# Kernel optimization log

Measured on AMD Instinct MI355X. Metric: run time of the kernel, lower is better.

## Reference

```python
import jax, jax.numpy as jnp
import numpy as np

B, T, D, H, F = 2, 2048, 1024, 16, 4096
DH = D // H  # 64
EPS = 1e-5


def setup_inputs() -> dict:
    key = jax.random.key(0)
    ks = jax.random.split(key, 12)
    s = 0.02
    return {
        "embedding": jax.random.normal(ks[0], (B, T, D), dtype=jnp.float32),
        "Wq": jax.random.normal(ks[1], (H, D, DH), dtype=jnp.float32) * s,
        "Wk": jax.random.normal(ks[2], (H, D, DH), dtype=jnp.float32) * s,
        "Wv": jax.random.normal(ks[3], (H, D, DH), dtype=jnp.float32) * s,
        "Wo": jax.random.normal(ks[4], (D, D), dtype=jnp.float32) * s,
        "bo": jnp.zeros((D,), dtype=jnp.float32),
        "W1": jax.random.normal(ks[5], (D, F), dtype=jnp.float32) * s,
        "b1": jnp.zeros((F,), dtype=jnp.float32),
        "W2": jax.random.normal(ks[6], (F, D), dtype=jnp.float32) * s,
        "b2": jnp.zeros((D,), dtype=jnp.float32),
        "g1": jnp.ones((D,), dtype=jnp.float32),
        "be1": jnp.zeros((D,), dtype=jnp.float32),
        "g2": jnp.ones((D,), dtype=jnp.float32),
        "be2": jnp.zeros((D,), dtype=jnp.float32),
    }


def _layernorm(x, g, b):
    mu = jnp.mean(x, axis=-1, keepdims=True)
    var = jnp.mean(jnp.square(x - mu), axis=-1, keepdims=True)
    return (x - mu) * jax.lax.rsqrt(var + EPS) * g + b


def reference(embedding, Wq, Wk, Wv, Wo, bo, W1, b1, W2, b2, g1, be1, g2, be2):
    x = embedding  # [B, T, D]
    # per-head projections (no bias), stacked: [B, H, T, DH]
    q = jnp.einsum("btd,hde->bhte", x, Wq)
    k = jnp.einsum("btd,hde->bhte", x, Wk)
    v = jnp.einsum("btd,hde->bhte", x, Wv)
    scores = jnp.einsum("bhte,bhse->bhts", q, k)  # [B, H, T, T]
    mask = jnp.tril(jnp.ones((T, T), dtype=bool))
    # Original masks to -inf first, then scales; -inf * scale = -inf, so this
    # equals softmax(scale * scores) on the causal support.
    scale = DH ** (-0.5)
    scores = jnp.where(mask, scores * scale, -jnp.inf)
    attn = jax.nn.softmax(scores, axis=-1)
    o = jnp.einsum("bhts,bhse->bthe", attn, v).reshape(B, T, D)  # head concat
    attn_out = o @ Wo + bo
    a = x + _layernorm(attn_out, g1, be1)  # residual uses original input
    f = jax.nn.relu(a @ W1 + b1) @ W2 + b2
    out = x + _layernorm(f, g2, be2)  # NOTE: residual from x, as in source
    return out
```

## Files before the change

kernel.cpp:

```cpp
#include <hip/hip_runtime.h>
#include <hip/hip_bf16.h>


#define Bq_ 2
#define T_ 2048
#define D_ 1024
#define H_ 16
#define DH_ 64
#define F_ 4096
#define N_ (Bq_ * T_)
#define EPS_ 1e-5f
#define KP 72

typedef __hip_bfloat16 bf16;
typedef unsigned short u16;
typedef __attribute__((ext_vector_type(8))) short bfrag;
typedef __attribute__((ext_vector_type(4))) float f32x4;

__device__ __forceinline__ u16 f2b(float f) {
    bf16 h = __float2bfloat16(f);
    return *(u16*)&h;
}
__device__ __forceinline__ float b2f_bits(u16 u) {
    return __uint_as_float(((unsigned)u) << 16);
}

__device__ __forceinline__ int swz(int row, int col) {
    return (col & ~31) | ((((col >> 3) ^ (row >> 1)) & 3) << 3) | (col & 7);
}

template <int N>
__device__ __forceinline__ void vmwait() {
    asm volatile("s_waitcnt vmcnt(%0)" :: "i"(N) : "memory");
}

#define GLDS16(g, l) __builtin_amdgcn_global_load_lds( \
    (const __attribute__((address_space(1))) unsigned int*)(g), \
    (__attribute__((address_space(3))) unsigned int*)(l), 16, 0, 0)

__device__ __forceinline__ void tc_body(
    float (*Ts)[65], const float* s, int spitch,
    u16* dst, int dpitch, int drow0, int kcol0)
{
    const int t = threadIdx.x;
    #pragma unroll
    for (int i = 0; i < 4; i++) {
        const int idx = t + i * 256;
        const int kk = idx >> 4;
        const int mm = (idx & 15) * 4;
        float4 v = *(const float4*)(s + (size_t)kk * spitch + mm);
        Ts[mm][kk] = v.x; Ts[mm + 1][kk] = v.y;
        Ts[mm + 2][kk] = v.z; Ts[mm + 3][kk] = v.w;
    }
    __syncthreads();
    const int mm = t >> 2;
    const int kk0 = (t & 3) * 16;
    u16 o[16];
    #pragma unroll
    for (int j = 0; j < 16; j++) o[j] = f2b(Ts[mm][kk0 + j]);
    const int dr = drow0 + mm;
    u16* drow = dst + (size_t)dr * dpitch;
    const int c0 = kcol0 + kk0;
    *(uint4*)&drow[swz(dr, c0)]     = *(uint4*)&o[0];
    *(uint4*)&drow[swz(dr, c0 + 8)] = *(uint4*)&o[8];
}

__global__ __launch_bounds__(256) void tcvt(
    const float* __restrict__ src, int spitch, int srow0, int scol0,
    u16* __restrict__ dst, int dpitch, int drow0)
{
    __shared__ float Ts[64][65];
    const int mb = blockIdx.x, kb = blockIdx.y;
    const float* s = src + (size_t)(srow0 + kb * 64) * spitch + scol0 + mb * 64;
    tc_body(Ts, s, spitch, dst, dpitch, drow0 + mb * 64, kb * 64);
}

__global__ __launch_bounds__(256) void tcvt_kv(
    const float* __restrict__ Wk, const float* __restrict__ Wv,
    u16* __restrict__ dst)
{
    __shared__ float Ts[64][65];
    const int kb = blockIdx.y, z = blockIdx.z;
    const int sel = z >> 4, zz = z & 15;
    const float* src = sel ? Wv : Wk;
    const float* s = src + (size_t)zz * 1024 * 64 + (size_t)(kb * 64) * 64;
    tc_body(Ts, s, 64, dst, 1024, sel * 1024 + zz * 64, kb * 64);
}

__global__ __launch_bounds__(256) void tcvt_ffn(
    const float* __restrict__ W1, const float* __restrict__ W2, int c,
    u16* __restrict__ W1T, u16* __restrict__ W2T)
{
    __shared__ float Ts[64][65];
    const int mb = blockIdx.x, kb = blockIdx.y, z = blockIdx.z;
    const float* src = z ? W2 : W1;
    const int spitch = z ? 1024 : 4096;
    const int srow0  = z ? c * 1024 : 0;
    const int scol0  = z ? 0 : c * 1024;
    u16* dst = z ? W2T : W1T;
    const float* s = src + (size_t)(srow0 + kb * 64) * spitch + scol0 + mb * 64;
    tc_body(Ts, s, spitch, dst, 1024, mb * 64, kb * 64);
}

template <int AF32, int SPLIT, int RELU, int ACC, int NT, int CSWZ, int WAVE>
__global__ __launch_bounds__(256) void cgemm(
    const void* __restrict__ A, int lda,
    const u16* __restrict__ BT,
    u16* __restrict__ C0, u16* __restrict__ C1, int ldc,
    int Kdim,
    const float* __restrict__ bias, int bias_off)
{
    static_assert(NT == 2 || NT == 4, "NT");
    static_assert(!AF32 || NT == 4, "AF32 path assumes BN=128");
    static_assert(!(AF32 && WAVE), "WAVE requires glds-only staging");
    constexpr int BN = NT * 32;
    constexpr int NBUF = (NT == 2) ? 5 : 4;
    constexpr int DPT  = NBUF - 1;
    constexpr int LPT  = 4 + NT;
    constexpr int BELEM = 64 * 32;
    constexpr int AELEM = NT * 16 * 32;
    constexpr int PBUF  = BELEM + AELEM;
    constexpr int SELEM = WAVE ? 4 * NBUF * PBUF
                               : 2 * BN * 32 + 2 * 128 * 32;
    __shared__ alignas(16) u16 SMEM[SELEM];

    const int tid = threadIdx.x;
    const int lane = tid & 63;
    const int w = tid >> 6;
    const int lo16 = lane & 15;
    const int quad = lane >> 4;
    const int wi = w >> 1, wj = w & 1;

    const int m0 = blockIdx.x * 128;
    const int n0 = blockIdx.y * BN;

    f32x4 acc[NT][4] = {};

    const int c8 = (lane & 3) * 8;
    const int r4 = lane >> 2;
    const int fcol = ((quad ^ ((lo16 >> 1) & 3)) << 3);

    const int nsteps = Kdim >> 5;

    if constexpr (WAVE) {
        const u16* Ab = (const u16*)A;
        u16* wbase = &SMEM[w * NBUF * PBUF];
        auto wstage = [&](int slot, int k0) {
            u16* bb = wbase + slot * PBUF;
            #pragma unroll
            for (int c = 0; c < 4; c++)
                GLDS16(BT + (size_t)(m0 + wj * 64 + c * 16 + r4) * Kdim + k0 + c8,
                       bb + c * 512);
            u16* ab = bb + BELEM;
            #pragma unroll
            for (int c = 0; c < NT; c++)
                GLDS16(Ab + (size_t)(n0 + wi * (NT * 16) + c * 16 + r4) * lda + k0 + c8,
                       ab + c * 512);
        };
        #pragma unroll
        for (int i = 0; i < DPT; i++) wstage(i, i * 32);
        int t = 0, cb = 0;
        for (; t + DPT <= nsteps; ++t) {
            vmwait<(DPT - 1) * LPT>();
            __builtin_amdgcn_sched_barrier(0);
            const u16* bb = wbase + cb * PBUF;
            const u16* ab = bb + BELEM;
            bfrag af[NT], bfv[4];
            #pragma unroll
            for (int it = 0; it < NT; it++)
                af[it] = *(const bfrag*)(ab + (it * 16 + lo16) * 32 + fcol);
            #pragma unroll
            for (int jt = 0; jt < 4; jt++)
                bfv[jt] = *(const bfrag*)(bb + (jt * 16 + lo16) * 32 + fcol);
            if (t + DPT < nsteps)
                wstage(cb == 0 ? NBUF - 1 : cb - 1, (t + DPT) * 32);
            __builtin_amdgcn_s_setprio(1);
            #pragma unroll
            for (int it = 0; it < NT; it++)
                #pragma unroll
                for (int jt = 0; jt < 4; jt++)
                    acc[it][jt] = __builtin_amdgcn_mfma_f32_16x16x32_bf16(
                        af[it], bfv[jt], acc[it][jt], 0, 0, 0);
            __builtin_amdgcn_s_setprio(0);
            cb = (cb + 1 == NBUF) ? 0 : cb + 1;
        }
        vmwait<0>();
        __builtin_amdgcn_sched_barrier(0);
        for (; t < nsteps; ++t) {
            const u16* bb = wbase + cb * PBUF;
            const u16* ab = bb + BELEM;
            bfrag af[NT], bfv[4];
            #pragma unroll
            for (int it = 0; it < NT; it++)
                af[it] = *(const bfrag*)(ab + (it * 16 + lo16) * 32 + fcol);
            #pragma unroll
            for (int jt = 0; jt < 4; jt++)
                bfv[jt] = *(const bfrag*)(bb + (jt * 16 + lo16) * 32 + fcol);
            #pragma unroll
            for (int it = 0; it < NT; it++)
                #pragma unroll
                for (int jt = 0; jt < 4; jt++)
                    acc[it][jt] = __builtin_amdgcn_mfma_f32_16x16x32_bf16(
                        af[it], bfv[jt], acc[it][jt], 0, 0, 0);
            cb = (cb + 1 == NBUF) ? 0 : cb + 1;
        }
    } else {
        u16* As_ = SMEM;
        u16* Bs_ = SMEM + 2 * BN * 32;
        const int br0 = w * 32 + r4;
        const int br1 = br0 + 16;
        auto stage = [&](int buf, int k0) {
            GLDS16(BT + (size_t)(m0 + br0) * Kdim + k0 + c8,
                   Bs_ + buf * 128 * 32 + (w * 2 + 0) * 512);
            GLDS16(BT + (size_t)(m0 + br1) * Kdim + k0 + c8,
                   Bs_ + buf * 128 * 32 + (w * 2 + 1) * 512);
            const int ar = tid >> 1;
            const int kh = (tid & 1) * 16;
            const float* ap = (const float*)A + (size_t)(n0 + ar) * lda + k0 + kh;
            float4 v0 = ((const float4*)ap)[0];
            float4 v1 = ((const float4*)ap)[1];
            float4 v2 = ((const float4*)ap)[2];
            float4 v3 = ((const float4*)ap)[3];
            uint4 a0, a1;
            a0.x = (unsigned)f2b(v0.x) | ((unsigned)f2b(v0.y) << 16);
            a0.y = (unsigned)f2b(v0.z) | ((unsigned)f2b(v0.w) << 16);
            a0.z = (unsigned)f2b(v1.x) | ((unsigned)f2b(v1.y) << 16);
            a0.w = (unsigned)f2b(v1.z) | ((unsigned)f2b(v1.w) << 16);
            a1.x = (unsigned)f2b(v2.x) | ((unsigned)f2b(v2.y) << 16);
            a1.y = (unsigned)f2b(v2.z) | ((unsigned)f2b(v2.w) << 16);
            a1.z = (unsigned)f2b(v3.x) | ((unsigned)f2b(v3.y) << 16);
            a1.w = (unsigned)f2b(v3.z) | ((unsigned)f2b(v3.w) << 16);
            u16* arow = As_ + buf * BN * 32 + ar * 32;
            *(uint4*)&arow[swz(ar, kh)] = a0;
            *(uint4*)&arow[swz(ar, kh + 8)] = a1;
        };
        stage(0, 0);
        __syncthreads();
        int cur = 0;
        for (int t = 0; t < nsteps; ++t) {
            if (t + 1 < nsteps) stage(cur ^ 1, (t + 1) * 32);
            bfrag af[NT], bfv[4];
            #pragma unroll
            for (int it = 0; it < NT; it++)
                af[it] = *(const bfrag*)(As_ + cur * BN * 32
                         + (wi * (NT * 16) + it * 16 + lo16) * 32 + fcol);
            #pragma unroll
            for (int jt = 0; jt < 4; jt++)
                bfv[jt] = *(const bfrag*)(Bs_ + cur * 128 * 32
                          + (wj * 64 + jt * 16 + lo16) * 32 + fcol);
            __builtin_amdgcn_s_setprio(1);
            #pragma unroll
            for (int it = 0; it < NT; it++)
                #pragma unroll
                for (int jt = 0; jt < 4; jt++)
                    acc[it][jt] = __builtin_amdgcn_mfma_f32_16x16x32_bf16(
                        af[it], bfv[jt], acc[it][jt], 0, 0, 0);
            __builtin_amdgcn_s_setprio(0);
            if (t + 1 < nsteps) {
                __syncthreads();
                cur ^= 1;
            }
        }
    }
    #pragma unroll
    for (int jt = 0; jt < 4; jt++) {
        const int col = m0 + wj * 64 + jt * 16 + lo16;
        u16* Cp;
        int cc;
        if constexpr (SPLIT) {
            Cp = (col >> 10) ? C1 : C0;
            cc = col & 1023;
        } else {
            Cp = C0;
            cc = col;
        }
        const float bv = bias ? bias[bias_off + col] : 0.f;
        #pragma unroll
        for (int it = 0; it < NT; it++) {
            #pragma unroll
            for (int r = 0; r < 4; r++) {
                const int row = n0 + wi * (NT * 16) + it * 16 + quad * 4 + r;
                float v = acc[it][jt][r] + bv;
                if constexpr (RELU) v = fmaxf(v, 0.f);
                const int ccs = CSWZ ? swz(row, cc) : cc;
                u16* cp = Cp + (size_t)row * ldc + ccs;
                if constexpr (ACC) v += b2f_bits(*cp);
                *cp = f2b(v);
            }
        }
    }
}

template <int AF32, int QKV, int RELU, int ACC>
__global__ __launch_bounds__(256) void mgemm(
    const void* __restrict__ A,
    const float* __restrict__ B0f, const float* __restrict__ B1f, const float* __restrict__ B2f,
    u16* __restrict__ C0, u16* __restrict__ C1, u16* __restrict__ C2,
    int ldb, int brow_off, int bcol_off,
    const float* __restrict__ bias, int bias_off)
{
    __shared__ alignas(16) u16 As[128][32];
    __shared__ alignas(16) u16 Bt[128][40];
    __shared__ alignas(16) float Bs32[32][132];

    const int tid = threadIdx.x;
    const int lane = tid & 63;
    const int w = tid >> 6;
    const int lo16 = lane & 15;
    const int quad = lane >> 4;
    const int wi = w >> 1, wj = w & 1;

    const int m0 = blockIdx.x * 128;
    const int n0 = blockIdx.y * 128;

    f32x4 acc[4][4] = {};

    const int ar  = tid >> 1;
    const int akh = (tid & 1) * 16;
    const int bmq = tid & 31;
    const int bkb = (tid >> 5) * 4;
    const int tm  = tid >> 1;
    const int tkh = (tid & 1) * 16;

    for (int k0 = 0; k0 < 1024; k0 += 32) {
        uint4 a0, a1;
        if constexpr (AF32) {
            const float* ap = (const float*)A + (size_t)(n0 + ar) * 1024 + k0 + akh;
            float4 v0 = ((const float4*)ap)[0];
            float4 v1 = ((const float4*)ap)[1];
            float4 v2 = ((const float4*)ap)[2];
            float4 v3 = ((const float4*)ap)[3];
            a0.x = (unsigned)f2b(v0.x) | ((unsigned)f2b(v0.y) << 16);
            a0.y = (unsigned)f2b(v0.z) | ((unsigned)f2b(v0.w) << 16);
            a0.z = (unsigned)f2b(v1.x) | ((unsigned)f2b(v1.y) << 16);
            a0.w = (unsigned)f2b(v1.z) | ((unsigned)f2b(v1.w) << 16);
            a1.x = (unsigned)f2b(v2.x) | ((unsigned)f2b(v2.y) << 16);
            a1.y = (unsigned)f2b(v2.z) | ((unsigned)f2b(v2.w) << 16);
            a1.z = (unsigned)f2b(v3.x) | ((unsigned)f2b(v3.y) << 16);
            a1.w = (unsigned)f2b(v3.z) | ((unsigned)f2b(v3.w) << 16);
        } else {
            const u16* ap = (const u16*)A + (size_t)(n0 + ar) * 1024 + k0 + akh;
            a0 = ((const uint4*)ap)[0];
            a1 = ((const uint4*)ap)[1];
        }
        #pragma unroll
        for (int kk = 0; kk < 4; kk++) {
            const int k = bkb + kk;
            const float* bp;
            if constexpr (QKV) {
                const int m = m0 + bmq * 4;
                const int sel = m >> 10;
                const int mm = m & 1023;
                const float* Wp = (sel == 0) ? B0f : ((sel == 1) ? B1f : B2f);
                bp = Wp + ((size_t)(mm >> 6) * 1024 + k0 + k) * 64 + (mm & 63);
            } else {
                bp = B0f + (size_t)(brow_off + k0 + k) * ldb + bcol_off + m0 + bmq * 4;
            }
            *(float4*)&Bs32[k][bmq * 4] = *(const float4*)bp;
        }
        __syncthreads();
        *(uint4*)&As[ar][akh] = a0;
        *(uint4*)&As[ar][akh + 8] = a1;
        {
            u16 t[16];
            #pragma unroll
            for (int i = 0; i < 16; i++) t[i] = f2b(Bs32[tkh + i][tm]);
            *(uint4*)&Bt[tm][tkh] = *(uint4*)&t[0];
            *(uint4*)&Bt[tm][tkh + 8] = *(uint4*)&t[8];
        }
        __syncthreads();
        bfrag af[4], bfv[4];
        #pragma unroll
        for (int it = 0; it < 4; it++)
            af[it] = *(const bfrag*)&As[wi * 64 + it * 16 + lo16][quad * 8];
        #pragma unroll
        for (int jt = 0; jt < 4; jt++)
            bfv[jt] = *(const bfrag*)&Bt[wj * 64 + jt * 16 + lo16][quad * 8];
        #pragma unroll
        for (int it = 0; it < 4; it++)
            #pragma unroll
            for (int jt = 0; jt < 4; jt++)
                acc[it][jt] = __builtin_amdgcn_mfma_f32_16x16x32_bf16(
                    af[it], bfv[jt], acc[it][jt], 0, 0, 0);
        __syncthreads();
    }
    #pragma unroll
    for (int jt = 0; jt < 4; jt++) {
        const int col = m0 + wj * 64 + jt * 16 + lo16;
        u16* Cp;
        int cc;
        if constexpr (QKV) {
            const int sel = col >> 10;
            cc = col & 1023;
            Cp = (sel == 0) ? C0 : ((sel == 1) ? C1 : C2);
        } else {
            Cp = C0;
            cc = col;
        }
        const float bv = bias ? bias[bias_off + col] : 0.f;
        #pragma unroll
        for (int it = 0; it < 4; it++) {
            #pragma unroll
            for (int r = 0; r < 4; r++) {
                const int row = n0 + wi * 64 + it * 16 + quad * 4 + r;
                float v = acc[it][jt][r] + bv;
                if constexpr (RELU) v = fmaxf(v, 0.f);
                u16* cp = Cp + (size_t)row * 1024 + cc;
                if constexpr (ACC) v += b2f_bits(*cp);
                *cp = f2b(v);
            }
        }
    }
}

__global__ __launch_bounds__(256) void fattn_kernel(
    u16* __restrict__ Q, const u16* __restrict__ Kg, const u16* __restrict__ Vg)
{
    const int bo_ = blockIdx.x;
    const int bi = ((bo_ & 7) << 6) | (bo_ >> 3);
    const int qp = bi & 15;
    const int h  = (bi >> 4) & 15;
    const int b  = bi >> 8;
    const int tid = threadIdx.x;
    const int w = tid >> 6;
    const int lane = tid & 63;
    const int lo16 = lane & 15;
    const int quad = lane >> 4;

    __shared__ alignas(16) u16 Ks[64][KP];
    __shared__ alignas(16) u16 Vt[64][KP];
    __shared__ alignas(16) u16 Ps[4][16][KP];

    const int sr = tid >> 2;
    const int ec = (tid & 3) * 16;

    #pragma unroll 1
    for (int pi = 0; pi < 2; pi++) {
        const int qt = pi ? (31 - qp) : qp;
        const int q0 = qt * 64;
        const size_t qrow = (size_t)(b * T_ + q0 + w * 16 + lo16) * 1024 + h * 64;
        bfrag qa0 = *(const bfrag*)(Q + qrow + quad * 8);
        bfrag qa1 = *(const bfrag*)(Q + qrow + 32 + quad * 8);

        f32x4 oacc[4] = {};
        float m_r[4], l_r[4];
        #pragma unroll
        for (int r = 0; r < 4; r++) { m_r[r] = -3e38f; l_r[r] = 0.f; }

        uint4 ka, kb, va, vb;
        {
            const size_t grow = (size_t)(b * T_ + sr) * 1024 + h * 64 + ec;
            ka = *(const uint4*)(Kg + grow);
            kb = *(const uint4*)(Kg + grow + 8);
            va = *(const uint4*)(Vg + grow);
            vb = *(const uint4*)(Vg + grow + 8);
        }

        for (int st = 0; st <= qt; st++) {
            *(uint4*)&Ks[sr][ec] = ka;
            *(uint4*)&Ks[sr][ec + 8] = kb;
            {
                unsigned vv[8] = {va.x, va.y, va.z, va.w, vb.x, vb.y, vb.z, vb.w};
                #pragma unroll
                for (int k2 = 0; k2 < 8; k2++) {
                    Vt[ec + 2 * k2][sr]     = (u16)(vv[k2] & 0xffff);
                    Vt[ec + 2 * k2 + 1][sr] = (u16)(vv[k2] >> 16);
                }
            }
            __syncthreads();
            if (st < qt) {
                const size_t grow = (size_t)(b * T_ + (st + 1) * 64 + sr) * 1024
                                  + h * 64 + ec;
                ka = *(const uint4*)(Kg + grow);
                kb = *(const uint4*)(Kg + grow + 8);
                va = *(const uint4*)(Vg + grow);
                vb = *(const uint4*)(Vg + grow + 8);
            }

            float sv[4][4];
            #pragma unroll
            for (int nt = 0; nt < 4; nt++) {
                bfrag kb0 = *(const bfrag*)&Ks[nt * 16 + lo16][quad * 8];
                bfrag kb1 = *(const bfrag*)&Ks[nt * 16 + lo16][32 + quad * 8];
                f32x4 cs = {0.f, 0.f, 0.f, 0.f};
                cs = __builtin_amdgcn_mfma_f32_16x16x32_bf16(qa0, kb0, cs, 0, 0, 0);
                cs = __builtin_amdgcn_mfma_f32_16x16x32_bf16(qa1, kb1, cs, 0, 0, 0);
                #pragma unroll
                for (int r = 0; r < 4; r++) sv[nt][r] = cs[r] * 0.125f;
            }
            if (st == qt) {
                #pragma unroll
                for (int nt = 0; nt < 4; nt++)
                    #pragma unroll
                    for (int r = 0; r < 4; r++)
                        if (nt * 16 + lo16 > w * 16 + quad * 4 + r) sv[nt][r] = -3e38f;
            }
            #pragma unroll
            for (int r = 0; r < 4; r++) {
                float m = fmaxf(fmaxf(sv[0][r], sv[1][r]), fmaxf(sv[2][r], sv[3][r]));
                #pragma unroll
                for (int off = 1; off < 16; off <<= 1)
                    m = fmaxf(m, __shfl_xor(m, off, 64));
                float mnew = fmaxf(m_r[r], m);
                float alpha = __expf(m_r[r] - mnew);
                m_r[r] = mnew;
                float s = 0.f;
                #pragma unroll
                for (int nt = 0; nt < 4; nt++) {
                    sv[nt][r] = __expf(sv[nt][r] - mnew);
                    s += sv[nt][r];
                }
                #pragma unroll
                for (int off = 1; off < 16; off <<= 1)
                    s += __shfl_xor(s, off, 64);
                l_r[r] = l_r[r] * alpha + s;
                #pragma unroll
                for (int et = 0; et < 4; et++) oacc[et][r] *= alpha;
            }
            #pragma unroll
            for (int nt = 0; nt < 4; nt++)
                #pragma unroll
                for (int r = 0; r < 4; r++)
                    Ps[w][quad * 4 + r][nt * 16 + lo16] = f2b(sv[nt][r]);
            bfrag pa0 = *(const bfrag*)&Ps[w][lo16][quad * 8];
            bfrag pa1 = *(const bfrag*)&Ps[w][lo16][32 + quad * 8];
            #pragma unroll
            for (int et = 0; et < 4; et++) {
                bfrag vb0 = *(const bfrag*)&Vt[et * 16 + lo16][quad * 8];
                bfrag vb1 = *(const bfrag*)&Vt[et * 16 + lo16][32 + quad * 8];
                oacc[et] = __builtin_amdgcn_mfma_f32_16x16x32_bf16(pa0, vb0, oacc[et], 0, 0, 0);
                oacc[et] = __builtin_amdgcn_mfma_f32_16x16x32_bf16(pa1, vb1, oacc[et], 0, 0, 0);
            }
            __syncthreads();
        }
        #pragma unroll
        for (int r = 0; r < 4; r++) {
            float rl = 1.f / l_r[r];
            const int row = q0 + w * 16 + quad * 4 + r;
            u16* orow = Q + (size_t)(b * T_ + row) * 1024;
            #pragma unroll
            for (int et = 0; et < 4; et++)
                orow[swz(row, h * 64 + et * 16 + lo16)] = f2b(oacc[et][r] * rl);
        }
    }
}

template <int WF32, int OSWZ>
__global__ __launch_bounds__(256) void ln_kernel(
    const u16* __restrict__ src, const float* __restrict__ resid,
    const float* __restrict__ g, const float* __restrict__ be,
    u16* __restrict__ dstb, float* __restrict__ dstf)
{
    const int r = blockIdx.x;
    const int tid = threadIdx.x;
    uint2 raw = ((const uint2*)(src + (size_t)r * D_))[tid];
    float y[4];
    y[0] = __uint_as_float(raw.x << 16);
    y[1] = __uint_as_float(raw.x & 0xffff0000u);
    y[2] = __uint_as_float(raw.y << 16);
    y[3] = __uint_as_float(raw.y & 0xffff0000u);
    float s = y[0] + y[1] + y[2] + y[3];
    float sq = y[0]*y[0] + y[1]*y[1] + y[2]*y[2] + y[3]*y[3];
    #pragma unroll
    for (int o = 32; o > 0; o >>= 1) {
        s += __shfl_down(s, o, 64);
        sq += __shfl_down(sq, o, 64);
    }
    __shared__ float rs[4], rq[4];
    if ((tid & 63) == 0) { rs[tid >> 6] = s; rq[tid >> 6] = sq; }
    __syncthreads();
    const float S = rs[0] + rs[1] + rs[2] + rs[3];
    const float Qm = rq[0] + rq[1] + rq[2] + rq[3];
    const float mu = S * (1.f / (float)D_);
    const float var = fmaxf(Qm * (1.f / (float)D_) - mu * mu, 0.f);
    const float rstd = rsqrtf(var + EPS_);
    const int c = tid * 4;
    #pragma unroll
    for (int i = 0; i < 4; i++) {
        y[i] = (y[i] - mu) * rstd * g[c + i] + be[c + i]
             + resid[(size_t)r * D_ + c + i];
    }
    if constexpr (WF32) {
        float4 o = {y[0], y[1], y[2], y[3]};
        ((float4*)(dstf + (size_t)r * D_))[tid] = o;
    } else {
        uint2 o;
        o.x = (unsigned)f2b(y[0]) | ((unsigned)f2b(y[1]) << 16);
        o.y = (unsigned)f2b(y[2]) | ((unsigned)f2b(y[3]) << 16);
        const int cs = OSWZ ? swz(r, c) : c;
        *(uint2*)(dstb + (size_t)r * D_ + cs) = o;
    }
}

extern "C" void kernel_launch(void* const* d_in, const int* in_sizes, int n_in,
                              void* d_out, int out_size, void* d_ws, size_t ws_size,
                              hipStream_t stream)
{
    const float* emb = (const float*)d_in[0];
    const float* Wq  = (const float*)d_in[1];
    const float* Wk  = (const float*)d_in[2];
    const float* Wv  = (const float*)d_in[3];
    const float* Wo  = (const float*)d_in[4];
    const float* bo  = (const float*)d_in[5];
    const float* W1  = (const float*)d_in[6];
    const float* b1  = (const float*)d_in[7];
    const float* W2  = (const float*)d_in[8];
    const float* b2  = (const float*)d_in[9];
    const float* g1  = (const float*)d_in[10];
    const float* be1 = (const float*)d_in[11];
    const float* g2  = (const float*)d_in[12];
    const float* be2 = (const float*)d_in[13];

    u16* WS = (u16*)d_ws;
    u16* DO = (u16*)d_out;

    const size_t M1 = 1024 * 1024;
    u16* WkvT = WS;
    u16* Q    = WS;
    u16* Kb   = DO;
    u16* Vb   = DO + 4 * M1;
    u16* O    = WS;
    u16* WoT  = DO;
    u16* P    = DO + 4 * M1;
    u16* Af   = DO;
    u16* Hc   = DO + 4 * M1;
    u16* W1T  = DO + 6 * M1;
    u16* W2T  = DO + 7 * M1;
    u16* F    = WS;
    float* outf = (float*)d_out;

    const dim3 blk(256);

    tcvt_kv<<<dim3(1, 16, 32), blk, 0, stream>>>(Wk, Wv, WkvT);
    cgemm<1, 1, 0, 0, 4, 0, 0><<<dim3(16, 32), blk, 0, stream>>>(
        emb, 1024, WkvT, Kb, Vb, 1024, 1024, nullptr, 0);
    mgemm<1, 1, 0, 0><<<dim3(8, 32), blk, 0, stream>>>(
        emb, Wq, Wq, Wq, Q, nullptr, nullptr, 0, 0, 0, nullptr, 0);
    fattn_kernel<<<Bq_ * H_ * 16, blk, 0, stream>>>(Q, Kb, Vb);
    tcvt<<<dim3(16, 16), blk, 0, stream>>>(Wo, 1024, 0, 0, WoT, 1024, 0);
    cgemm<0, 0, 0, 0, 4, 0, 1><<<dim3(8, 32), blk, 0, stream>>>(
        O, 1024, WoT, P, nullptr, 1024, 1024, bo, 0);
    ln_kernel<0, 1><<<N_, blk, 0, stream>>>(P, emb, g1, be1, Af, nullptr);
    for (int c = 0; c < 4; c++) {
        tcvt_ffn<<<dim3(16, 16, 2), blk, 0, stream>>>(W1, W2, c, W1T, W2T);
        for (int rh = 0; rh < 2; rh++) {
            u16* Afh = Af + (size_t)rh * 2048 * 1024;
            u16* Fh  = F  + (size_t)rh * 2048 * 1024;
            cgemm<0, 0, 1, 0, 2, 1, 1><<<dim3(8, 32), blk, 0, stream>>>(
                Afh, 1024, W1T, Hc, nullptr, 1024, 1024, b1, c * 1024);
            if (c == 0) {
                cgemm<0, 0, 0, 0, 2, 0, 1><<<dim3(8, 32), blk, 0, stream>>>(
                    Hc, 1024, W2T, Fh, nullptr, 1024, 1024, b2, 0);
            } else {
                cgemm<0, 0, 0, 1, 2, 0, 1><<<dim3(8, 32), blk, 0, stream>>>(
                    Hc, 1024, W2T, Fh, nullptr, 1024, 1024, nullptr, 0);
            }
        }
    }
    ln_kernel<1, 0><<<N_, blk, 0, stream>>>(F, emb, g2, be2, nullptr, outf);
}
```

Baseline: 558.5 us.

## Share K/V tiles across paired query tiles and remap GEMM blocks per XCD

The attention kernel previously handled its two paired query tiles (qp and 31-qp) one after the other, loading the K/V prefix twice. It now runs one loop over the longer prefix and processes both query tiles against each staged K/V tile, so the shorter tile's K/V loads are shared. This roughly halves K/V global traffic and LDS staging for those steps, at the cost of more live registers for two accumulator sets. Separately, both GEMM kernels remap block indices so consecutive blocks dispatched to the same XCD cover neighbouring tiles, aiming for better L2 locality.

```diff
diff --git a/kernel.cpp b/kernel.cpp
--- a/kernel.cpp
+++ b/kernel.cpp
@@ -37,6 +37,13 @@
 #define GLDS16(g, l) __builtin_amdgcn_global_load_lds( \
     (const __attribute__((address_space(1))) unsigned int*)(g), \
     (__attribute__((address_space(3))) unsigned int*)(l), 16, 0, 0)
+
+__device__ __forceinline__ void xcd_remap(int gx, int& bx, int& by) {
+    const int bid = blockIdx.x + gx * blockIdx.y;
+    const int t8 = bid >> 3;
+    bx = t8 % gx;
+    by = (bid & 7) + 8 * (t8 / gx);
+}
 
 __device__ __forceinline__ void tc_body(
     float (*Ts)[65], const float* s, int spitch,
@@ -131,8 +138,10 @@
     const int quad = lane >> 4;
     const int wi = w >> 1, wj = w & 1;
 
-    const int m0 = blockIdx.x * 128;
-    const int n0 = blockIdx.y * BN;
+    int bx, by;
+    xcd_remap(gridDim.x, bx, by);
+    const int m0 = bx * 128;
+    const int n0 = by * BN;
 
     f32x4 acc[NT][4] = {};
 
@@ -310,8 +319,10 @@
     const int quad = lane >> 4;
     const int wi = w >> 1, wj = w & 1;
 
-    const int m0 = blockIdx.x * 128;
-    const int n0 = blockIdx.y * 128;
+    int bx, by;
+    xcd_remap(gridDim.x, bx, by);
+    const int m0 = bx * 128;
+    const int n0 = by * 128;
 
     f32x4 acc[4][4] = {};
 
@@ -434,113 +445,124 @@
     const int sr = tid >> 2;
     const int ec = (tid & 3) * 16;
 
-    #pragma unroll 1
-    for (int pi = 0; pi < 2; pi++) {
-        const int qt = pi ? (31 - qp) : qp;
-        const int q0 = qt * 64;
-        const size_t qrow = (size_t)(b * T_ + q0 + w * 16 + lo16) * 1024 + h * 64;
-        bfrag qa0 = *(const bfrag*)(Q + qrow + quad * 8);
-        bfrag qa1 = *(const bfrag*)(Q + qrow + 32 + quad * 8);
-
-        f32x4 oacc[4] = {};
-        float m_r[4], l_r[4];
-        #pragma unroll
-        for (int r = 0; r < 4; r++) { m_r[r] = -3e38f; l_r[r] = 0.f; }
-
-        uint4 ka, kb, va, vb;
+    const int qtA = qp, qtB = 31 - qp;
+
+    const size_t qrowA = (size_t)(b * T_ + qtA * 64 + w * 16 + lo16) * 1024 + h * 64;
+    const size_t qrowB = (size_t)(b * T_ + qtB * 64 + w * 16 + lo16) * 1024 + h * 64;
+    bfrag qaA0 = *(const bfrag*)(Q + qrowA + quad * 8);
+    bfrag qaA1 = *(const bfrag*)(Q + qrowA + 32 + quad * 8);
+    bfrag qaB0 = *(const bfrag*)(Q + qrowB + quad * 8);
+    bfrag qaB1 = *(const bfrag*)(Q + qrowB + 32 + quad * 8);
+
+    f32x4 oaccA[4] = {}, oaccB[4] = {};
+    float mA[4], lA[4], mB[4], lB[4];
+    #pragma unroll
+    for (int r = 0; r < 4; r++) { mA[r] = mB[r] = -3e38f; lA[r] = lB[r] = 0.f; }
+
+    uint4 ka, kb, va, vb;
+    {
+        const size_t grow = (size_t)(b * T_ + sr) * 1024 + h * 64 + ec;
+        ka = *(const uint4*)(Kg + grow);
+        kb = *(const uint4*)(Kg + grow + 8);
+        va = *(const uint4*)(Vg + grow);
+        vb = *(const uint4*)(Vg + grow + 8);
+    }
+
+    auto proc = [&](bfrag q0f, bfrag q1f, f32x4* oacc, float* m_r, float* l_r,
+                    int qt, int st) {
+        float sv[4][4];
+        #pragma unroll
+        for (int nt = 0; nt < 4; nt++) {
+            bfrag kb0 = *(const bfrag*)&Ks[nt * 16 + lo16][quad * 8];
+            bfrag kb1 = *(const bfrag*)&Ks[nt * 16 + lo16][32 + quad * 8];
+            f32x4 cs = {0.f, 0.f, 0.f, 0.f};
+            cs = __builtin_amdgcn_mfma_f32_16x16x32_bf16(q0f, kb0, cs, 0, 0, 0);
+            cs = __builtin_amdgcn_mfma_f32_16x16x32_bf16(q1f, kb1, cs, 0, 0, 0);
+            #pragma unroll
+            for (int r = 0; r < 4; r++) sv[nt][r] = cs[r] * 0.125f;
+        }
+        if (st == qt) {
+            #pragma unroll
+            for (int nt = 0; nt < 4; nt++)
+                #pragma unroll
+                for (int r = 0; r < 4; r++)
+                    if (nt * 16 + lo16 > w * 16 + quad * 4 + r) sv[nt][r] = -3e38f;
+        }
+        #pragma unroll
+        for (int r = 0; r < 4; r++) {
+            float m = fmaxf(fmaxf(sv[0][r], sv[1][r]), fmaxf(sv[2][r], sv[3][r]));
+            #pragma unroll
+            for (int off = 1; off < 16; off <<= 1)
+                m = fmaxf(m, __shfl_xor(m, off, 64));
+            float mnew = fmaxf(m_r[r], m);
+            float alpha = __expf(m_r[r] - mnew);
+            m_r[r] = mnew;
+            float s = 0.f;
+            #pragma unroll
+            for (int nt = 0; nt < 4; nt++) {
+                sv[nt][r] = __expf(sv[nt][r] - mnew);
+                s += sv[nt][r];
+            }
+            #pragma unroll
+            for (int off = 1; off < 16; off <<= 1)
+                s += __shfl_xor(s, off, 64);
+            l_r[r] = l_r[r] * alpha + s;
+            #pragma unroll
+            for (int et = 0; et < 4; et++) oacc[et][r] *= alpha;
+        }
+        #pragma unroll
+        for (int nt = 0; nt < 4; nt++)
+            #pragma unroll
+            for (int r = 0; r < 4; r++)
+                Ps[w][quad * 4 + r][nt * 16 + lo16] = f2b(sv[nt][r]);
+        bfrag pa0 = *(const bfrag*)&Ps[w][lo16][quad * 8];
+        bfrag pa1 = *(const bfrag*)&Ps[w][lo16][32 + quad * 8];
+        #pragma unroll
+        for (int et = 0; et < 4; et++) {
+            bfrag vb0 = *(const bfrag*)&Vt[et * 16 + lo16][quad * 8];
+            bfrag vb1 = *(const bfrag*)&Vt[et * 16 + lo16][32 + quad * 8];
+            oacc[et] = __builtin_amdgcn_mfma_f32_16x16x32_bf16(pa0, vb0, oacc[et], 0, 0, 0);
+            oacc[et] = __builtin_amdgcn_mfma_f32_16x16x32_bf16(pa1, vb1, oacc[et], 0, 0, 0);
+        }
+    };
+
+    for (int st = 0; st <= qtB; st++) {
+        *(uint4*)&Ks[sr][ec] = ka;
+        *(uint4*)&Ks[sr][ec + 8] = kb;
         {
-            const size_t grow = (size_t)(b * T_ + sr) * 1024 + h * 64 + ec;
+            unsigned vv[8] = {va.x, va.y, va.z, va.w, vb.x, vb.y, vb.z, vb.w};
+            #pragma unroll
+            for (int k2 = 0; k2 < 8; k2++) {
+                Vt[ec + 2 * k2][sr]     = (u16)(vv[k2] & 0xffff);
+                Vt[ec + 2 * k2 + 1][sr] = (u16)(vv[k2] >> 16);
+            }
+        }
+        __syncthreads();
+        if (st < qtB) {
+            const size_t grow = (size_t)(b * T_ + (st + 1) * 64 + sr) * 1024
+                              + h * 64 + ec;
             ka = *(const uint4*)(Kg + grow);
             kb = *(const uint4*)(Kg + grow + 8);
             va = *(const uint4*)(Vg + grow);
             vb = *(const uint4*)(Vg + grow + 8);
         }
-
-        for (int st = 0; st <= qt; st++) {
-            *(uint4*)&Ks[sr][ec] = ka;
-            *(uint4*)&Ks[sr][ec + 8] = kb;
-            {
-                unsigned vv[8] = {va.x, va.y, va.z, va.w, vb.x, vb.y, vb.z, vb.w};
-                #pragma unroll
-                for (int k2 = 0; k2 < 8; k2++) {
-                    Vt[ec + 2 * k2][sr]     = (u16)(vv[k2] & 0xffff);
-                    Vt[ec + 2 * k2 + 1][sr] = (u16)(vv[k2] >> 16);
-                }
-            }
-            __syncthreads();
-            if (st < qt) {
-                const size_t grow = (size_t)(b * T_ + (st + 1) * 64 + sr) * 1024
-                                  + h * 64 + ec;
-                ka = *(const uint4*)(Kg + grow);
-                kb = *(const uint4*)(Kg + grow + 8);
-                va = *(const uint4*)(Vg + grow);
-                vb = *(const uint4*)(Vg + grow + 8);
-            }
-
-            float sv[4][4];
-            #pragma unroll
-            for (int nt = 0; nt < 4; nt++) {
-                bfrag kb0 = *(const bfrag*)&Ks[nt * 16 + lo16][quad * 8];
-                bfrag kb1 = *(const bfrag*)&Ks[nt * 16 + lo16][32 + quad * 8];
-                f32x4 cs = {0.f, 0.f, 0.f, 0.f};
-                cs = __builtin_amdgcn_mfma_f32_16x16x32_bf16(qa0, kb0, cs, 0, 0, 0);
-                cs = __builtin_amdgcn_mfma_f32_16x16x32_bf16(qa1, kb1, cs, 0, 0, 0);
-                #pragma unroll
-                for (int r = 0; r < 4; r++) sv[nt][r] = cs[r] * 0.125f;
-            }
-            if (st == qt) {
-                #pragma unroll
-                for (int nt = 0; nt < 4; nt++)
-                    #pragma unroll
-                    for (int r = 0; r < 4; r++)
-                        if (nt * 16 + lo16 > w * 16 + quad * 4 + r) sv[nt][r] = -3e38f;
-            }
-            #pragma unroll
-            for (int r = 0; r < 4; r++) {
-                float m = fmaxf(fmaxf(sv[0][r], sv[1][r]), fmaxf(sv[2][r], sv[3][r]));
-                #pragma unroll
-                for (int off = 1; off < 16; off <<= 1)
-                    m = fmaxf(m, __shfl_xor(m, off, 64));
-                float mnew = fmaxf(m_r[r], m);
-                float alpha = __expf(m_r[r] - mnew);
-                m_r[r] = mnew;
-                float s = 0.f;
-                #pragma unroll
-                for (int nt = 0; nt < 4; nt++) {
-                    sv[nt][r] = __expf(sv[nt][r] - mnew);
-                    s += sv[nt][r];
-                }
-                #pragma unroll
-                for (int off = 1; off < 16; off <<= 1)
-                    s += __shfl_xor(s, off, 64);
-                l_r[r] = l_r[r] * alpha + s;
-                #pragma unroll
-                for (int et = 0; et < 4; et++) oacc[et][r] *= alpha;
-            }
-            #pragma unroll
-            for (int nt = 0; nt < 4; nt++)
-                #pragma unroll
-                for (int r = 0; r < 4; r++)
-                    Ps[w][quad * 4 + r][nt * 16 + lo16] = f2b(sv[nt][r]);
-            bfrag pa0 = *(const bfrag*)&Ps[w][lo16][quad * 8];
-            bfrag pa1 = *(const bfrag*)&Ps[w][lo16][32 + quad * 8];
-            #pragma unroll
-            for (int et = 0; et < 4; et++) {
-                bfrag vb0 = *(const bfrag*)&Vt[et * 16 + lo16][quad * 8];
-                bfrag vb1 = *(const bfrag*)&Vt[et * 16 + lo16][32 + quad * 8];
-                oacc[et] = __builtin_amdgcn_mfma_f32_16x16x32_bf16(pa0, vb0, oacc[et], 0, 0, 0);
-                oacc[et] = __builtin_amdgcn_mfma_f32_16x16x32_bf16(pa1, vb1, oacc[et], 0, 0, 0);
-            }
-            __syncthreads();
-        }
-        #pragma unroll
-        for (int r = 0; r < 4; r++) {
-            float rl = 1.f / l_r[r];
-            const int row = q0 + w * 16 + quad * 4 + r;
-            u16* orow = Q + (size_t)(b * T_ + row) * 1024;
-            #pragma unroll
-            for (int et = 0; et < 4; et++)
-                orow[swz(row, h * 64 + et * 16 + lo16)] = f2b(oacc[et][r] * rl);
+        proc(qaB0, qaB1, oaccB, mB, lB, qtB, st);
+        if (st <= qtA)
+            proc(qaA0, qaA1, oaccA, mA, lA, qtA, st);
+        __syncthreads();
+    }
+    #pragma unroll
+    for (int r = 0; r < 4; r++) {
+        float rlA = 1.f / lA[r];
+        float rlB = 1.f / lB[r];
+        const int rowA = qtA * 64 + w * 16 + quad * 4 + r;
+        const int rowB = qtB * 64 + w * 16 + quad * 4 + r;
+        u16* orowA = Q + (size_t)(b * T_ + rowA) * 1024;
+        u16* orowB = Q + (size_t)(b * T_ + rowB) * 1024;
+        #pragma unroll
+        for (int et = 0; et < 4; et++) {
+            orowA[swz(rowA, h * 64 + et * 16 + lo16)] = f2b(oaccA[et][r] * rlA);
+            orowB[swz(rowB, h * 64 + et * 16 + lo16)] = f2b(oaccB[et][r] * rlB);
         }
     }
 }
```

After: 547.6 us. No clear change (-1.9%).
